# Kernel optimization log

Measured on AMD Instinct MI355X. Metric: run time of the kernel, lower is better.

The kernel has to match this reference:

```python
import jax, jax.numpy as jnp
import numpy as np

HIDDEN = 512
NUM_HEADS = 8
HEAD_DIM = HIDDEN // NUM_HEADS
B, S = 4, 2048


def setup_inputs() -> dict:
    key = jax.random.key(0)
    ks = jax.random.split(key, 10)
    p = lambda k, shape: (jax.random.normal(k, shape, dtype=jnp.float32) * 0.02)
    return {
        "lstm_output": jax.random.normal(ks[0], (B, S, HIDDEN), dtype=jnp.float32),
        "padding_mask": jax.random.randint(ks[1], (S,), 0, 2, dtype=jnp.int32),
        "Wq": p(ks[2], (HIDDEN, HIDDEN)), "bq": p(ks[3], (HIDDEN,)),
        "Wk": p(ks[4], (HIDDEN, HIDDEN)), "bk": p(ks[5], (HIDDEN,)),
        "Wv": p(ks[6], (HIDDEN, HIDDEN)), "bv": p(ks[7], (HIDDEN,)),
        "Wo": p(ks[8], (HIDDEN, HIDDEN)), "bo": p(ks[9], (HIDDEN,)),
    }


def reference(lstm_output, padding_mask, Wq, bq, Wk, bk, Wv, bv, Wo, bo):
    b, s, hid = lstm_output.shape
    # QKV projections (torch Linear: x @ W.T + b)
    q = lstm_output @ Wq.T + bq
    k = lstm_output @ Wk.T + bk
    v = lstm_output @ Wv.T + bv
    # Faithful to source: direct row-major reshape (B,S,H*hd) -> (B*H, S, hd)
    q = q.reshape(b * NUM_HEADS, -1, HEAD_DIM)
    k = k.reshape(b * NUM_HEADS, -1, HEAD_DIM)
    v = v.reshape(b * NUM_HEADS, -1, HEAD_DIM)
    # Scores scaled by sqrt(hidden_size), as in source (not sqrt(head_dim))
    score = jnp.einsum('bqd,bkd->bqk', q, k) / jnp.sqrt(jnp.float32(hid))
    # mask (S,) -> broadcast over key axis; masked_fill(mask==0, -inf)
    score = jnp.where(padding_mask[None, None, :] == 0, -jnp.inf, score)
    attn = jax.nn.softmax(score, axis=-1)
    wv = jnp.einsum('bqk,bkd->bqd', attn, v)          # (B*H, S, hd)
    wv = jnp.swapaxes(wv, 1, 2).reshape(b, -1, hid)    # transpose(1,2).view(B,-1,hid)
    return wv @ Wo.T + bo
```

## Files before the change

### kernel.cpp

```cpp
#include <hip/hip_runtime.h>
#include <hip/hip_bf16.h>

#define HID 512
#define SEQ 2048
#define NG 32
#define HD 64
#define MROWS 8192
#define LDP 72
#define QSC 0.0637587178f
#define IDXN 2304

typedef __bf16 bf16x8 __attribute__((ext_vector_type(8)));
typedef float f32x4 __attribute__((ext_vector_type(4)));

#define MFMA(a, b, c) __builtin_amdgcn_mfma_f32_16x16x32_bf16((a), (b), (c), 0, 0, 0)

__global__ __launch_bounds__(256) void mask_scan(const int* __restrict__ mask,
                                                 int* __restrict__ hdr) {
    __shared__ int s[256];
    const int tid = threadIdx.x;
    const int base = tid * 8;
    int loc[8], cnt = 0;
    for (int j = 0; j < 8; ++j) { loc[j] = cnt; cnt += (mask[base + j] != 0); }
    s[tid] = cnt;
    __syncthreads();
    for (int off = 1; off < 256; off <<= 1) {
        int v = (tid >= off) ? s[tid - off] : 0;
        __syncthreads();
        s[tid] += v;
        __syncthreads();
    }
    const int excl = s[tid] - cnt;
    const int nvalid = s[255];
    int* idx = hdr + 1;
    int* cidx = hdr + 1 + IDXN;
    for (int j = 0; j < 8; ++j) {
        int i = base + j;
        bool v = (mask[i] != 0);
        cidx[i] = v ? (excl + loc[j]) : -1;
        if (v) idx[excl + loc[j]] = i;
    }
    if (tid == 0) hdr[0] = nvalid;
    __syncthreads();
    for (int p = nvalid + tid; p < IDXN; p += 256) idx[p] = 0;
}

__global__ __launch_bounds__(256) void vt_pad(__hip_bfloat16* __restrict__ vT,
                                              const int* __restrict__ hdr) {
    const int nvalid = hdr[0];
    const int cend = (nvalid + 63) & ~63;
    if (cend == nvalid) return;
    const int g = blockIdx.x;
    const __hip_bfloat16 z = (__hip_bfloat16)0.0f;
    for (int d = 0; d < HD; ++d)
        for (int c = nvalid + threadIdx.x; c < cend; c += 256)
            vT[(size_t)g * (HD * SEQ) + (size_t)d * SEQ + c] = z;
}

__global__ __launch_bounds__(256) void conv_x(const float* __restrict__ src,
                                              __hip_bfloat16* __restrict__ dst, int n4) {
    int stride = gridDim.x * 256;
    for (int i = blockIdx.x * 256 + threadIdx.x; i < n4; i += stride) {
        float4 v = *(const float4*)(src + (size_t)i * 4);
        union { __hip_bfloat16 h[4]; uint2 u; } p;
        p.h[0] = __float2bfloat16(v.x); p.h[1] = __float2bfloat16(v.y);
        p.h[2] = __float2bfloat16(v.z); p.h[3] = __float2bfloat16(v.w);
        *(uint2*)(dst + (size_t)i * 4) = p.u;
    }
}

__global__ __launch_bounds__(256) void conv_w(const float* __restrict__ a,
                                              const float* __restrict__ b,
                                              const float* __restrict__ c,
                                              const float* __restrict__ d,
                                              __hip_bfloat16* __restrict__ out) {
    int which = blockIdx.y;
    const float* s = which == 0 ? a : (which == 1 ? b : (which == 2 ? c : d));
    __hip_bfloat16* o = out + (size_t)which * (HID * HID);
    int i = blockIdx.x * 256 + threadIdx.x;
    float4 v = *(const float4*)(s + (size_t)i * 4);
    union { __hip_bfloat16 h[4]; uint2 u; } p;
    p.h[0] = __float2bfloat16(v.x); p.h[1] = __float2bfloat16(v.y);
    p.h[2] = __float2bfloat16(v.z); p.h[3] = __float2bfloat16(v.w);
    *(uint2*)(o + (size_t)i * 4) = p.u;
}

__global__ __launch_bounds__(256) void gemm_qkv_fused(
        const __hip_bfloat16* __restrict__ Xb,
        const __hip_bfloat16* __restrict__ Wqb, const __hip_bfloat16* __restrict__ Wkb,
        const __hip_bfloat16* __restrict__ Wvb,
        const float* __restrict__ bq, const float* __restrict__ bk, const float* __restrict__ bv,
        const int* __restrict__ hdr,
        __hip_bfloat16* __restrict__ qout, __hip_bfloat16* __restrict__ kout,
        __hip_bfloat16* __restrict__ vT) {
    __shared__ __hip_bfloat16 Xs[64][LDP];
    __shared__ __hip_bfloat16 Wqs[64][LDP];
    __shared__ __hip_bfloat16 Wks[64][LDP];
    __shared__ __hip_bfloat16 Wvs[64][LDP];
    const int tid = threadIdx.x;
    const int w = tid >> 6, l = tid & 63;
    const int h = l >> 4, q = l & 15;
    const int row0 = blockIdx.x * 64, col0 = blockIdx.y * 64;

    const int r0 = tid >> 3, r1 = (tid + 256) >> 3;
    const int cc0 = (tid & 7) * 8;
    uint4 px0, px1, pq0, pq1, pk0, pk1, pv0, pv1;
    {
        px0 = *(const uint4*)(Xb  + (size_t)(row0 + r0) * HID + cc0);
        px1 = *(const uint4*)(Xb  + (size_t)(row0 + r1) * HID + cc0);
        pq0 = *(const uint4*)(Wqb + (size_t)(col0 + r0) * HID + cc0);
        pq1 = *(const uint4*)(Wqb + (size_t)(col0 + r1) * HID + cc0);
        pk0 = *(const uint4*)(Wkb + (size_t)(col0 + r0) * HID + cc0);
        pk1 = *(const uint4*)(Wkb + (size_t)(col0 + r1) * HID + cc0);
        pv0 = *(const uint4*)(Wvb + (size_t)(col0 + r0) * HID + cc0);
        pv1 = *(const uint4*)(Wvb + (size_t)(col0 + r1) * HID + cc0);
    }

    f32x4 aq[4] = {}, ak[4] = {}, av[4] = {};
    for (int kt = 0; kt < 8; ++kt) {
        __syncthreads();
        *(uint4*)&Xs[r0][cc0]  = px0;  *(uint4*)&Xs[r1][cc0]  = px1;
        *(uint4*)&Wqs[r0][cc0] = pq0;  *(uint4*)&Wqs[r1][cc0] = pq1;
        *(uint4*)&Wks[r0][cc0] = pk0;  *(uint4*)&Wks[r1][cc0] = pk1;
        *(uint4*)&Wvs[r0][cc0] = pv0;  *(uint4*)&Wvs[r1][cc0] = pv1;
        __syncthreads();
        if (kt < 7) {
            size_t go = (size_t)(kt + 1) * 64 + cc0;
            px0 = *(const uint4*)(Xb  + (size_t)(row0 + r0) * HID + go);
            px1 = *(const uint4*)(Xb  + (size_t)(row0 + r1) * HID + go);
            pq0 = *(const uint4*)(Wqb + (size_t)(col0 + r0) * HID + go);
            pq1 = *(const uint4*)(Wqb + (size_t)(col0 + r1) * HID + go);
            pk0 = *(const uint4*)(Wkb + (size_t)(col0 + r0) * HID + go);
            pk1 = *(const uint4*)(Wkb + (size_t)(col0 + r1) * HID + go);
            pv0 = *(const uint4*)(Wvb + (size_t)(col0 + r0) * HID + go);
            pv1 = *(const uint4*)(Wvb + (size_t)(col0 + r1) * HID + go);
        }
        for (int dk = 0; dk < 2; ++dk) {
            bf16x8 x = *(const bf16x8*)&Xs[w * 16 + q][dk * 32 + 8 * h];
            for (int nt = 0; nt < 4; ++nt) {
                int rr = nt * 16 + q, cc = dk * 32 + 8 * h;
                aq[nt] = MFMA(*(const bf16x8*)&Wqs[rr][cc], x, aq[nt]);
                ak[nt] = MFMA(*(const bf16x8*)&Wks[rr][cc], x, ak[nt]);
                av[nt] = MFMA(*(const bf16x8*)&Wvs[rr][cc], x, av[nt]);
            }
        }
    }
    const int m = row0 + w * 16 + q;
    const int g = row0 >> 8;
    const int irow = ((m & 255) << 3) + (int)blockIdx.y;
    const int ci = hdr[1 + IDXN + irow];
    for (int nt = 0; nt < 4; ++nt) {
        int nb = col0 + nt * 16 + 4 * h;
        float4 b4q = *(const float4*)(bq + nb);
        float4 b4k = *(const float4*)(bk + nb);
        float4 b4v = *(const float4*)(bv + nb);
        const float* bqf = (const float*)&b4q;
        const float* bkf = (const float*)&b4k;
        const float* bvf = (const float*)&b4v;
        union { __hip_bfloat16 hh[4]; uint2 u; } oq, ok;
        for (int jj = 0; jj < 4; ++jj) {
            oq.hh[jj] = __float2bfloat16((aq[nt][jj] + bqf[jj]) * QSC);
            ok.hh[jj] = __float2bfloat16(ak[nt][jj] + bkf[jj]);
        }
        *(uint2*)(qout + (size_t)m * HID + nb) = oq.u;
        *(uint2*)(kout + (size_t)m * HID + nb) = ok.u;
        if (ci >= 0) {
            int db = nb & 63;
            for (int jj = 0; jj < 4; ++jj)
                vT[(size_t)g * (HD * SEQ) + (size_t)(db + jj) * SEQ + ci] =
                    __float2bfloat16(av[nt][jj] + bvf[jj]);
        }
    }
}

__global__ __launch_bounds__(256) void gemm_out(const __hip_bfloat16* __restrict__ X,
                                                const __hip_bfloat16* __restrict__ W,
                                                const float* __restrict__ bias,
                                                float* __restrict__ out) {
    __shared__ __hip_bfloat16 Xs[64][LDP];
    __shared__ __hip_bfloat16 Ws[64][LDP];
    const int tid = threadIdx.x;
    const int w = tid >> 6, l = tid & 63;
    const int h = l >> 4, q = l & 15;
    const int row0 = blockIdx.x * 64, col0 = blockIdx.y * 64;

    const int r0 = tid >> 3, r1 = (tid + 256) >> 3;
    const int cc0 = (tid & 7) * 8;
    uint4 px0 = *(const uint4*)(X + (size_t)(row0 + r0) * HID + cc0);
    uint4 px1 = *(const uint4*)(X + (size_t)(row0 + r1) * HID + cc0);
    uint4 pw0 = *(const uint4*)(W + (size_t)(col0 + r0) * HID + cc0);
    uint4 pw1 = *(const uint4*)(W + (size_t)(col0 + r1) * HID + cc0);

    f32x4 acc[4] = {};
    for (int kt = 0; kt < 8; ++kt) {
        __syncthreads();
        *(uint4*)&Xs[r0][cc0] = px0;  *(uint4*)&Xs[r1][cc0] = px1;
        *(uint4*)&Ws[r0][cc0] = pw0;  *(uint4*)&Ws[r1][cc0] = pw1;
        __syncthreads();
        if (kt < 7) {
            size_t go = (size_t)(kt + 1) * 64 + cc0;
            px0 = *(const uint4*)(X + (size_t)(row0 + r0) * HID + go);
            px1 = *(const uint4*)(X + (size_t)(row0 + r1) * HID + go);
            pw0 = *(const uint4*)(W + (size_t)(col0 + r0) * HID + go);
            pw1 = *(const uint4*)(W + (size_t)(col0 + r1) * HID + go);
        }
        for (int dk = 0; dk < 2; ++dk) {
            bf16x8 x = *(const bf16x8*)&Xs[w * 16 + q][dk * 32 + 8 * h];
            for (int nt = 0; nt < 4; ++nt) {
                bf16x8 b = *(const bf16x8*)&Ws[nt * 16 + q][dk * 32 + 8 * h];
                acc[nt] = MFMA(b, x, acc[nt]);
            }
        }
    }
    const int m = row0 + w * 16 + q;
    for (int nt = 0; nt < 4; ++nt) {
        int nb = col0 + nt * 16 + 4 * h;
        float4 b4 = *(const float4*)(bias + nb);
        float4 o = make_float4(acc[nt][0] + b4.x, acc[nt][1] + b4.y,
                               acc[nt][2] + b4.z, acc[nt][3] + b4.w);
        *(float4*)(out + (size_t)m * HID + nb) = o;
    }
}

__global__ __launch_bounds__(256) void attn(const __hip_bfloat16* __restrict__ qg,
                                            const __hip_bfloat16* __restrict__ kg,
                                            const __hip_bfloat16* __restrict__ vT,
                                            const int* __restrict__ hdr,
                                            __hip_bfloat16* __restrict__ wvt) {
    __shared__ __hip_bfloat16 Ks[2][64][LDP];
    __shared__ __hip_bfloat16 VTs[2][64][LDP];
    __shared__ float sb[2][64];

    const int tid = threadIdx.x;
    const int w = tid >> 6, l = tid & 63;
    const int h = l >> 4, q = l & 15;
    const int bid = (blockIdx.x & 7) * 64 + (blockIdx.x >> 3);
    const int g = bid >> 4, qt = bid & 15;
    const size_t hb = (size_t)g * (SEQ * HD);

    const int nvalid = hdr[0];
    const int ntiles = (nvalid + 63) >> 6;
    const int* idx = hdr + 1;

    bf16x8 qf[2][2];
    for (int m = 0; m < 2; ++m)
        for (int dk = 0; dk < 2; ++dk)
            qf[m][dk] = *(const bf16x8*)(qg + hb +
                (size_t)(qt * 128 + w * 32 + m * 16 + q) * HD + dk * 32 + 8 * h);

    const int r0 = tid >> 3, r1 = (tid + 256) >> 3;
    const int cc0 = (tid & 7) * 8;
    const int ntc = cc0 >> 4;
    const int cA = (ntc & 1) * 32 + ((cc0 >> 2) & 3) * 8 + (ntc >> 1) * 4;

    const __bf16 kOne = (__bf16)1.0f;
    const bf16x8 ones = {kOne, kOne, kOne, kOne, kOne, kOne, kOne, kOne};

    f32x4 acc[2][4] = {};
    f32x4 lsum[2] = {};

    uint4 kp0 = *(const uint4*)(kg + hb + (size_t)idx[r0] * HD + cc0);
    uint4 kp1 = *(const uint4*)(kg + hb + (size_t)idx[r1] * HD + cc0);
    uint4 vp0 = *(const uint4*)(vT + hb + (size_t)r0 * SEQ + cc0);
    uint4 vp1 = *(const uint4*)(vT + hb + (size_t)r1 * SEQ + cc0);

    *(uint4*)&Ks[0][r0][cc0] = kp0;
    *(uint4*)&Ks[0][r1][cc0] = kp1;
    *(uint2*)&VTs[0][r0][cA]     = make_uint2(vp0.x, vp0.y);
    *(uint2*)&VTs[0][r0][cA + 8] = make_uint2(vp0.z, vp0.w);
    *(uint2*)&VTs[0][r1][cA]     = make_uint2(vp1.x, vp1.y);
    *(uint2*)&VTs[0][r1][cA + 8] = make_uint2(vp1.z, vp1.w);
    if (tid < 64) sb[0][tid] = (tid < nvalid) ? 0.f : -1e38f;

    kp0 = *(const uint4*)(kg + hb + (size_t)idx[64 + r0] * HD + cc0);
    kp1 = *(const uint4*)(kg + hb + (size_t)idx[64 + r1] * HD + cc0);
    vp0 = *(const uint4*)(vT + hb + (size_t)r0 * SEQ + 64 + cc0);
    vp1 = *(const uint4*)(vT + hb + (size_t)r1 * SEQ + 64 + cc0);
    float sbpre = (64 + tid < nvalid) ? 0.f : -1e38f;
    __syncthreads();

    for (int kt = 0; kt < ntiles; ++kt) {
        const int cur = kt & 1;
        if (kt < ntiles - 1) {
            *(uint4*)&Ks[cur ^ 1][r0][cc0] = kp0;
            *(uint4*)&Ks[cur ^ 1][r1][cc0] = kp1;
            *(uint2*)&VTs[cur ^ 1][r0][cA]     = make_uint2(vp0.x, vp0.y);
            *(uint2*)&VTs[cur ^ 1][r0][cA + 8] = make_uint2(vp0.z, vp0.w);
            *(uint2*)&VTs[cur ^ 1][r1][cA]     = make_uint2(vp1.x, vp1.y);
            *(uint2*)&VTs[cur ^ 1][r1][cA + 8] = make_uint2(vp1.z, vp1.w);
            if (tid < 64) sb[cur ^ 1][tid] = sbpre;
        }
        if (kt < ntiles - 2) {
            const int tn = (kt + 2) * 64;
            kp0 = *(const uint4*)(kg + hb + (size_t)idx[tn + r0] * HD + cc0);
            kp1 = *(const uint4*)(kg + hb + (size_t)idx[tn + r1] * HD + cc0);
            vp0 = *(const uint4*)(vT + hb + (size_t)r0 * SEQ + tn + cc0);
            vp1 = *(const uint4*)(vT + hb + (size_t)r1 * SEQ + tn + cc0);
            sbpre = (tn + tid < nvalid) ? 0.f : -1e38f;
        }

        f32x4 sacc[2][4];
        for (int nt = 0; nt < 4; ++nt) {
            f32x4 binit = *(const f32x4*)&sb[cur][nt * 16 + 4 * h];
            sacc[0][nt] = binit;
            sacc[1][nt] = binit;
        }
        for (int dk = 0; dk < 2; ++dk) {
            for (int nt = 0; nt < 4; ++nt) {
                bf16x8 kf = *(const bf16x8*)&Ks[cur][nt * 16 + q][dk * 32 + 8 * h];
                sacc[0][nt] = MFMA(kf, qf[0][dk], sacc[0][nt]);
                sacc[1][nt] = MFMA(kf, qf[1][dk], sacc[1][nt]);
            }
        }
        union pk_t { bf16x8 v; __hip_bfloat16 hh[8]; } pa[2][2];
        for (int m = 0; m < 2; ++m)
            for (int kk = 0; kk < 2; ++kk)
                for (int j = 0; j < 4; ++j) {
                    pa[m][kk].hh[j]     = __float2bfloat16(exp2f(sacc[m][kk][j]));
                    pa[m][kk].hh[j + 4] = __float2bfloat16(exp2f(sacc[m][kk + 2][j]));
                }
        for (int kk = 0; kk < 2; ++kk) {
            lsum[0] = MFMA(pa[0][kk].v, ones, lsum[0]);
            lsum[1] = MFMA(pa[1][kk].v, ones, lsum[1]);
            for (int dt = 0; dt < 4; ++dt) {
                bf16x8 bv = *(const bf16x8*)&VTs[cur][dt * 16 + q][kk * 32 + 8 * h];
                acc[0][dt] = MFMA(pa[0][kk].v, bv, acc[0][dt]);
                acc[1][dt] = MFMA(pa[1][kk].v, bv, acc[1][dt]);
            }
        }
        __syncthreads();
    }

    for (int m = 0; m < 2; ++m) {
        float rinv[4];
        for (int jj = 0; jj < 4; ++jj) rinv[jj] = 1.f / lsum[m][jj];
        const int ibase = qt * 128 + w * 32 + m * 16 + 4 * h;
        for (int dt = 0; dt < 4; ++dt) {
            int d = dt * 16 + q;
            union { __hip_bfloat16 hh[4]; uint2 u; } o;
            for (int jj = 0; jj < 4; ++jj)
                o.hh[jj] = __float2bfloat16(acc[m][dt][jj] * rinv[jj]);
            *(uint2*)(wvt + (size_t)g * (HD * SEQ) + (size_t)d * SEQ + ibase) = o.u;
        }
    }
}

extern "C" void kernel_launch(void* const* d_in, const int* in_sizes, int n_in,
                              void* d_out, int out_size, void* d_ws, size_t ws_size,
                              hipStream_t stream) {
    const float* lstm = (const float*)d_in[0];
    const int* mask = (const int*)d_in[1];
    const float* Wq = (const float*)d_in[2]; const float* bq = (const float*)d_in[3];
    const float* Wk = (const float*)d_in[4]; const float* bk = (const float*)d_in[5];
    const float* Wv = (const float*)d_in[6]; const float* bv = (const float*)d_in[7];
    const float* Wo = (const float*)d_in[8]; const float* bo = (const float*)d_in[9];
    float* out = (float*)d_out;

    const size_t NX = (size_t)MROWS * HID;
    const size_t NW = (size_t)HID * HID;
    __hip_bfloat16* Xb  = (__hip_bfloat16*)d_ws;
    __hip_bfloat16* Wqb = Xb + NX;
    __hip_bfloat16* Wkb = Wqb + NW;
    __hip_bfloat16* Wvb = Wkb + NW;
    __hip_bfloat16* Wob = Wvb + NW;
    __hip_bfloat16* qb  = Wob + NW;
    __hip_bfloat16* kb  = qb + NX;
    int*            hdr = (int*)(kb + NX);
    __hip_bfloat16* vT  = (__hip_bfloat16*)d_out;
    __hip_bfloat16* wvt = Xb;

    mask_scan<<<1, 256, 0, stream>>>(mask, hdr);
    conv_x<<<2048, 256, 0, stream>>>(lstm, Xb, (int)(NX / 4));
    conv_w<<<dim3(256, 4), 256, 0, stream>>>(Wq, Wk, Wv, Wo, Wqb);

    dim3 gg(MROWS / 64, HID / 64), bb(256);
    gemm_qkv_fused<<<gg, bb, 0, stream>>>(Xb, Wqb, Wkb, Wvb, bq, bk, bv, hdr, qb, kb, vT);
    vt_pad<<<dim3(NG), bb, 0, stream>>>(vT, hdr);
    attn<<<dim3(NG * (SEQ / 128)), bb, 0, stream>>>(qb, kb, vT, hdr, wvt);
    gemm_out<<<gg, bb, 0, stream>>>(wvt, Wob, bo, out);
}
```

Before: 98.48 us.

## Compact valid K rows in QKV epilogue and merge conversion kernels

The QKV GEMM epilogue now writes K only for unmasked positions, into a per-head compacted buffer (like V^T already was). The attention kernel then loads K tiles contiguously instead of gathering through the index list, and the padding kernel also zeroes the tail of compacted K. The separate X and weight conversion kernels are merged into one launch. This removes the indirect index loads and the K writes for masked rows, at the cost of scattered row writes in the epilogue.

New measurement: 99.96 us. No clear change (+1.5%).

```diff
diff --git a/kernel.cpp b/kernel.cpp
--- a/kernel.cpp
+++ b/kernel.cpp
@@ -45,7 +45,8 @@
     for (int p = nvalid + tid; p < IDXN; p += 256) idx[p] = 0;
 }
 
-__global__ __launch_bounds__(256) void vt_pad(__hip_bfloat16* __restrict__ vT,
+__global__ __launch_bounds__(256) void kv_pad(__hip_bfloat16* __restrict__ vT,
+                                              __hip_bfloat16* __restrict__ kc,
                                               const int* __restrict__ hdr) {
     const int nvalid = hdr[0];
     const int cend = (nvalid + 63) & ~63;
@@ -55,34 +56,40 @@
     for (int d = 0; d < HD; ++d)
         for (int c = nvalid + threadIdx.x; c < cend; c += 256)
             vT[(size_t)g * (HD * SEQ) + (size_t)d * SEQ + c] = z;
-}
-
-__global__ __launch_bounds__(256) void conv_x(const float* __restrict__ src,
-                                              __hip_bfloat16* __restrict__ dst, int n4) {
-    int stride = gridDim.x * 256;
-    for (int i = blockIdx.x * 256 + threadIdx.x; i < n4; i += stride) {
-        float4 v = *(const float4*)(src + (size_t)i * 4);
+    const int ne = (cend - nvalid) * HD;
+    __hip_bfloat16* kp = kc + ((size_t)g * SEQ + nvalid) * HD;
+    for (int e = threadIdx.x; e < ne; e += 256) kp[e] = z;
+}
+
+__global__ __launch_bounds__(256) void prep(const float* __restrict__ X,
+                                            const float* __restrict__ Wq,
+                                            const float* __restrict__ Wk,
+                                            const float* __restrict__ Wv,
+                                            const float* __restrict__ Wo,
+                                            __hip_bfloat16* __restrict__ Xb,
+                                            __hip_bfloat16* __restrict__ Wc) {
+    const int b = blockIdx.x;
+    if (b < 2048) {
+        const int n4 = (MROWS * HID) / 4;
+        for (int i = b * 256 + threadIdx.x; i < n4; i += 2048 * 256) {
+            float4 v = *(const float4*)(X + (size_t)i * 4);
+            union { __hip_bfloat16 h[4]; uint2 u; } p;
+            p.h[0] = __float2bfloat16(v.x); p.h[1] = __float2bfloat16(v.y);
+            p.h[2] = __float2bfloat16(v.z); p.h[3] = __float2bfloat16(v.w);
+            *(uint2*)(Xb + (size_t)i * 4) = p.u;
+        }
+    } else {
+        const int wb = b - 2048;
+        const int which = wb >> 8;
+        const float* s = which == 0 ? Wq : (which == 1 ? Wk : (which == 2 ? Wv : Wo));
+        __hip_bfloat16* o = Wc + (size_t)which * (HID * HID);
+        const int i = (wb & 255) * 256 + threadIdx.x;
+        float4 v = *(const float4*)(s + (size_t)i * 4);
         union { __hip_bfloat16 h[4]; uint2 u; } p;
         p.h[0] = __float2bfloat16(v.x); p.h[1] = __float2bfloat16(v.y);
         p.h[2] = __float2bfloat16(v.z); p.h[3] = __float2bfloat16(v.w);
-        *(uint2*)(dst + (size_t)i * 4) = p.u;
-    }
-}
-
-__global__ __launch_bounds__(256) void conv_w(const float* __restrict__ a,
-                                              const float* __restrict__ b,
-                                              const float* __restrict__ c,
-                                              const float* __restrict__ d,
-                                              __hip_bfloat16* __restrict__ out) {
-    int which = blockIdx.y;
-    const float* s = which == 0 ? a : (which == 1 ? b : (which == 2 ? c : d));
-    __hip_bfloat16* o = out + (size_t)which * (HID * HID);
-    int i = blockIdx.x * 256 + threadIdx.x;
-    float4 v = *(const float4*)(s + (size_t)i * 4);
-    union { __hip_bfloat16 h[4]; uint2 u; } p;
-    p.h[0] = __float2bfloat16(v.x); p.h[1] = __float2bfloat16(v.y);
-    p.h[2] = __float2bfloat16(v.z); p.h[3] = __float2bfloat16(v.w);
-    *(uint2*)(o + (size_t)i * 4) = p.u;
+        *(uint2*)(o + (size_t)i * 4) = p.u;
+    }
 }
 
 __global__ __launch_bounds__(256) void gemm_qkv_fused(
@@ -91,7 +98,7 @@
         const __hip_bfloat16* __restrict__ Wvb,
         const float* __restrict__ bq, const float* __restrict__ bk, const float* __restrict__ bv,
         const int* __restrict__ hdr,
-        __hip_bfloat16* __restrict__ qout, __hip_bfloat16* __restrict__ kout,
+        __hip_bfloat16* __restrict__ qout, __hip_bfloat16* __restrict__ kc,
         __hip_bfloat16* __restrict__ vT) {
     __shared__ __hip_bfloat16 Xs[64][LDP];
     __shared__ __hip_bfloat16 Wqs[64][LDP];
@@ -163,9 +170,9 @@
             ok.hh[jj] = __float2bfloat16(ak[nt][jj] + bkf[jj]);
         }
         *(uint2*)(qout + (size_t)m * HID + nb) = oq.u;
-        *(uint2*)(kout + (size_t)m * HID + nb) = ok.u;
         if (ci >= 0) {
             int db = nb & 63;
+            *(uint2*)(kc + ((size_t)g * SEQ + ci) * HD + db) = ok.u;
             for (int jj = 0; jj < 4; ++jj)
                 vT[(size_t)g * (HD * SEQ) + (size_t)(db + jj) * SEQ + ci] =
                     __float2bfloat16(av[nt][jj] + bvf[jj]);
@@ -223,7 +230,7 @@
 }
 
 __global__ __launch_bounds__(256) void attn(const __hip_bfloat16* __restrict__ qg,
-                                            const __hip_bfloat16* __restrict__ kg,
+                                            const __hip_bfloat16* __restrict__ kc,
                                             const __hip_bfloat16* __restrict__ vT,
                                             const int* __restrict__ hdr,
                                             __hip_bfloat16* __restrict__ wvt) {
@@ -240,7 +247,6 @@
 
     const int nvalid = hdr[0];
     const int ntiles = (nvalid + 63) >> 6;
-    const int* idx = hdr + 1;
 
     bf16x8 qf[2][2];
     for (int m = 0; m < 2; ++m)
@@ -259,8 +265,8 @@
     f32x4 acc[2][4] = {};
     f32x4 lsum[2] = {};
 
-    uint4 kp0 = *(const uint4*)(kg + hb + (size_t)idx[r0] * HD + cc0);
-    uint4 kp1 = *(const uint4*)(kg + hb + (size_t)idx[r1] * HD + cc0);
+    uint4 kp0 = *(const uint4*)(kc + hb + (size_t)r0 * HD + cc0);
+    uint4 kp1 = *(const uint4*)(kc + hb + (size_t)r1 * HD + cc0);
     uint4 vp0 = *(const uint4*)(vT + hb + (size_t)r0 * SEQ + cc0);
     uint4 vp1 = *(const uint4*)(vT + hb + (size_t)r1 * SEQ + cc0);
 
@@ -272,8 +278,8 @@
     *(uint2*)&VTs[0][r1][cA + 8] = make_uint2(vp1.z, vp1.w);
     if (tid < 64) sb[0][tid] = (tid < nvalid) ? 0.f : -1e38f;
 
-    kp0 = *(const uint4*)(kg + hb + (size_t)idx[64 + r0] * HD + cc0);
-    kp1 = *(const uint4*)(kg + hb + (size_t)idx[64 + r1] * HD + cc0);
+    kp0 = *(const uint4*)(kc + hb + (size_t)(64 + r0) * HD + cc0);
+    kp1 = *(const uint4*)(kc + hb + (size_t)(64 + r1) * HD + cc0);
     vp0 = *(const uint4*)(vT + hb + (size_t)r0 * SEQ + 64 + cc0);
     vp1 = *(const uint4*)(vT + hb + (size_t)r1 * SEQ + 64 + cc0);
     float sbpre = (64 + tid < nvalid) ? 0.f : -1e38f;
@@ -292,8 +298,8 @@
         }
         if (kt < ntiles - 2) {
             const int tn = (kt + 2) * 64;
-            kp0 = *(const uint4*)(kg + hb + (size_t)idx[tn + r0] * HD + cc0);
-            kp1 = *(const uint4*)(kg + hb + (size_t)idx[tn + r1] * HD + cc0);
+            kp0 = *(const uint4*)(kc + hb + (size_t)(tn + r0) * HD + cc0);
+            kp1 = *(const uint4*)(kc + hb + (size_t)(tn + r1) * HD + cc0);
             vp0 = *(const uint4*)(vT + hb + (size_t)r0 * SEQ + tn + cc0);
             vp1 = *(const uint4*)(vT + hb + (size_t)r1 * SEQ + tn + cc0);
             sbpre = (tn + tid < nvalid) ? 0.f : -1e38f;
@@ -364,18 +370,17 @@
     __hip_bfloat16* Wvb = Wkb + NW;
     __hip_bfloat16* Wob = Wvb + NW;
     __hip_bfloat16* qb  = Wob + NW;
-    __hip_bfloat16* kb  = qb + NX;
-    int*            hdr = (int*)(kb + NX);
+    __hip_bfloat16* kc  = qb + NX;
+    int*            hdr = (int*)(kc + NX);
     __hip_bfloat16* vT  = (__hip_bfloat16*)d_out;
     __hip_bfloat16* wvt = Xb;
 
     mask_scan<<<1, 256, 0, stream>>>(mask, hdr);
-    conv_x<<<2048, 256, 0, stream>>>(lstm, Xb, (int)(NX / 4));
-    conv_w<<<dim3(256, 4), 256, 0, stream>>>(Wq, Wk, Wv, Wo, Wqb);
+    prep<<<3072, 256, 0, stream>>>(lstm, Wq, Wk, Wv, Wo, Xb, Wqb);
 
     dim3 gg(MROWS / 64, HID / 64), bb(256);
-    gemm_qkv_fused<<<gg, bb, 0, stream>>>(Xb, Wqb, Wkb, Wvb, bq, bk, bv, hdr, qb, kb, vT);
-    vt_pad<<<dim3(NG), bb, 0, stream>>>(vT, hdr);
-    attn<<<dim3(NG * (SEQ / 128)), bb, 0, stream>>>(qb, kb, vT, hdr, wvt);
+    gemm_qkv_fused<<<gg, bb, 0, stream>>>(Xb, Wqb, Wkb, Wvb, bq, bk, bv, hdr, qb, kc, vT);
+    kv_pad<<<dim3(NG), bb, 0, stream>>>(vT, kc, hdr);
+    attn<<<dim3(NG * (SEQ / 128)), bb, 0, stream>>>(qb, kc, vT, hdr, wvt);
     gemm_out<<<gg, bb, 0, stream>>>(wvt, Wob, bo, out);
 }
```
